# Optimization experiments

Hardware: AMD Instinct MI355X
Metric: run time of the kernel (lower is better)

The kernel has to match this reference:

```python
import jax, jax.numpy as jnp
import numpy as np

B, C, D = 512, 50000, 256
N_LOADED = 40000


def setup_inputs() -> dict:
    key = jax.random.key(0)
    k1, k2, k3, k4 = jax.random.split(key, 4)
    visual_feats = jax.random.normal(k1, (B, D), dtype=jnp.float32)
    text_feats = jax.random.normal(k2, (C, D), dtype=jnp.float32)
    # sparse multi-hot labels; force class 0 positive for every row so the
    # positive set (intersected with loaded ids) is never empty
    batch_label = (jax.random.uniform(k3, (B, C)) < 0.02).astype(jnp.int32)
    batch_label = batch_label.at[:, 0].set(1)
    # distinct loaded class ids; force id 0 to be loaded
    ids = jax.random.permutation(k4, C)[:N_LOADED].astype(jnp.int32)
    ids = jnp.sort(ids).at[0].set(0)
    return {
        "visual_feats": visual_feats,
        "text_feats": text_feats,
        "batch_label": batch_label,
        "class_ids_loaded": ids,
        "d_space": D,
    }


def reference(visual_feats, text_feats, batch_label, class_ids_loaded, d_space):
    num_classes = text_feats.shape[0]
    # membership mask for loaded class ids (the set() intersection in torch)
    loaded = jnp.zeros((num_classes,), dtype=bool).at[class_ids_loaded].set(True)

    # cosine similarity; note: torch adds 1e-6 eps only to text-feature norms
    v = visual_feats / jnp.linalg.norm(visual_feats, axis=1, keepdims=True)
    t = text_feats / (1e-6 + jnp.linalg.norm(text_feats, axis=1, keepdims=True))
    S = v @ t.T  # [B, C]

    pos = (batch_label != 0) & loaded[None, :]  # ragged positive sets, as mask
    neg = (batch_label == 0) & loaded[None, :]  # ragged negative sets, as mask

    # denominator: sum of exp(sim) over negatives, per row
    denom = jnp.sum(jnp.where(neg, jnp.exp(S), 0.0), axis=1)  # [B]
    n_pos = jnp.sum(pos, axis=1).astype(S.dtype)  # [B]

    # per-row loss: mean over positives of -log(exp(s_p)/denom) = log(denom)-s_p
    per_row = jnp.sum(jnp.where(pos, jnp.log(denom)[:, None] - S, 0.0), axis=1) / n_pos
    return jnp.mean(per_row).reshape(1)
```

## Files before the change

### kernel.cpp

```cpp
#include <hip/hip_runtime.h>
#include <math.h>

#define D_DIM 256
#define GTM 64
#define GTN 64
#define BK 32
#define NB 782
#define NBP 784
#define CBPR 4
#define CBLKS (CBPR * 512)

typedef __attribute__((ext_vector_type(8))) short short8;
typedef __attribute__((ext_vector_type(4))) float floatx4;
typedef unsigned long long u64;

__device__ __forceinline__ unsigned short f2bf(float f) {
    unsigned int u = __float_as_uint(f);
    u += 0x7FFFu + ((u >> 16) & 1u);
    return (unsigned short)(u >> 16);
}

__device__ __forceinline__ void gload16(const void* g, void* lds) {
    __builtin_amdgcn_global_load_lds(
        (const __attribute__((address_space(1))) unsigned int*)g,
        (__attribute__((address_space(3))) unsigned int*)lds, 16, 0, 0);
}

__global__ __launch_bounds__(256) void prep_compress(
    const float* __restrict__ V, const float* __restrict__ T,
    const int* __restrict__ label, const int* __restrict__ ids,
    u64* __restrict__ loadedmask, u64* __restrict__ posmask,
    unsigned short* __restrict__ Vb, unsigned short* __restrict__ Tb,
    float* __restrict__ gaccum, unsigned int* __restrict__ gcount,
    int B, int C, int n_loaded, int WPR) {
    const int bid = blockIdx.x;
    const int tid = threadIdx.x;
    const int lane = tid & 63;

    if (bid < CBLKS) {
        __shared__ unsigned char nib[4096];
        int row = bid / CBPR;
        int sub = bid - row * CBPR;
        int cbase = sub * 16384;
        const int* lp = label + (size_t)row * C;
        int4 q[16];
        #pragma unroll
        for (int j = 0; j < 16; ++j) {
            int col = cbase + j * 1024 + tid * 4;
            if (col < C) q[j] = *(const int4*)(lp + col);
            else         q[j] = make_int4(0, 0, 0, 0);
        }
        #pragma unroll
        for (int j = 0; j < 16; ++j) {
            unsigned int n = (q[j].x ? 1u : 0u) | (q[j].y ? 2u : 0u) |
                             (q[j].z ? 4u : 0u) | (q[j].w ? 8u : 0u);
            nib[j * 256 + tid] = (unsigned char)n;
        }
        __syncthreads();
        #pragma unroll
        for (int h = 0; h < 2; ++h) {
            int widx = h * 256 + tid;
            u64 nb8 = *(const u64*)&nib[widx * 8];
            unsigned int word = 0;
            #pragma unroll
            for (int j = 0; j < 8; ++j)
                word |= ((unsigned int)((nb8 >> (8 * j)) & 0xFu)) << (4 * j);
            int u32idx = sub * 512 + widx;
            if (u32idx < 2 * WPR)
                ((unsigned int*)(posmask + (size_t)row * WPR))[u32idx] = word;
        }
        return;
    }

    int ptid = (bid - CBLKS) * 256 + tid;
    if (ptid == 0) { *gcount = 0u; *gaccum = 0.f; }
    if (ptid < WPR) {
        int base = ptid << 6;
        int lo = 0, hi = n_loaded;
        while (lo < hi) { int mid = (lo + hi) >> 1; if (ids[mid] < base) lo = mid + 1; else hi = mid; }
        u64 m = 0;
        for (int i = lo; i < n_loaded; ++i) {
            int v = ids[i]; if (v >= base + 64) break;
            m |= 1ull << (v - base);
        }
        loadedmask[ptid] = m;
    }
    int pwave = (bid - CBLKS) * 4 + (tid >> 6);
    int r0 = pwave * 4;
    if (r0 >= B + C) return;
    float4 x[4];
    #pragma unroll
    for (int q = 0; q < 4; ++q) {
        int wv = r0 + q;
        if (wv < B + C) {
            const float* src = (wv < B) ? (V + (size_t)wv * D_DIM)
                                        : (T + (size_t)(wv - B) * D_DIM);
            x[q] = ((const float4*)src)[lane];
        }
    }
    #pragma unroll
    for (int q = 0; q < 4; ++q) {
        int wv = r0 + q;
        if (wv >= B + C) break;
        bool isV = wv < B;
        float ss = x[q].x * x[q].x + x[q].y * x[q].y + x[q].z * x[q].z + x[q].w * x[q].w;
        #pragma unroll
        for (int off = 32; off > 0; off >>= 1) ss += __shfl_xor(ss, off);
        float nrm = sqrtf(ss);
        float s = isV ? (1.0f / nrm) : (1.0f / (1e-6f + nrm));
        ushort4 o;
        o.x = f2bf(x[q].x * s); o.y = f2bf(x[q].y * s);
        o.z = f2bf(x[q].z * s); o.w = f2bf(x[q].w * s);
        unsigned short* dst = isV ? (Vb + (size_t)wv * D_DIM)
                                  : (Tb + (size_t)(wv - B) * D_DIM);
        ((ushort4*)dst)[lane] = o;
    }
}

__global__ __launch_bounds__(256) void gemm_fused(
    const unsigned short* __restrict__ Vb, const unsigned short* __restrict__ Tb,
    const u64* __restrict__ posmask, const u64* __restrict__ loadedmask,
    float* __restrict__ denomP, float* __restrict__ posP, int C, int WPR) {
    __shared__ unsigned short As[GTM * BK];
    __shared__ unsigned short Bs[GTN * BK];
    __shared__ float sDen[GTM], sPos[GTM];

    const int tid  = threadIdx.x;
    const int lane = tid & 63;
    const int w    = tid >> 6;
    const int m0 = blockIdx.x * GTM;
    const int n0 = blockIdx.y * GTN;

    if (tid < GTM) { sDen[tid] = 0.f; sPos[tid] = 0.f; }

    const int sra = lane >> 2;
    const int kc  = (lane & 3) * 8;
    int ga = m0 + w * 16 + sra;
    int gb = n0 + w * 16 + sra;
    if (gb >= C) gb = C - 1;
    const unsigned short* gA = Vb + (size_t)ga * D_DIM + kc;
    const unsigned short* gB = Tb + (size_t)gb * D_DIM + kc;
    unsigned short* lA = &As[w * 16 * BK];
    unsigned short* lB = &Bs[w * 16 * BK];

    const int wm = (w >> 1) * 32;
    const int wn = (w & 1) * 32;
    const int fr = lane & 15;
    const int quad = lane >> 4;

    floatx4 acc[2][2];
    #pragma unroll
    for (int mi = 0; mi < 2; mi++)
        #pragma unroll
        for (int ni = 0; ni < 2; ni++) acc[mi][ni] = (floatx4)0.f;

    #pragma unroll
    for (int kt = 0; kt < D_DIM / BK; ++kt) {
        if (kt) __syncthreads();
        gload16(gA + kt * BK, lA);
        gload16(gB + kt * BK, lB);
        __syncthreads();
        short8 af[2], bf[2];
        #pragma unroll
        for (int mi = 0; mi < 2; mi++)
            af[mi] = *(const short8*)&As[(wm + mi * 16 + fr) * BK + quad * 8];
        #pragma unroll
        for (int ni = 0; ni < 2; ni++)
            bf[ni] = *(const short8*)&Bs[(wn + ni * 16 + fr) * BK + quad * 8];
        #pragma unroll
        for (int mi = 0; mi < 2; mi++)
            #pragma unroll
            for (int ni = 0; ni < 2; ni++)
                acc[mi][ni] = __builtin_amdgcn_mfma_f32_16x16x32_bf16(
                    af[mi], bf[ni], acc[mi][ni], 0, 0, 0);
    }

    const int wordIdx = n0 >> 6;
    const u64 loadedw = loadedmask[wordIdx];
    #pragma unroll
    for (int mi = 0; mi < 2; mi++) {
        #pragma unroll
        for (int i = 0; i < 4; i++) {
            const int mloc = wm + mi * 16 + quad * 4 + i;
            const u64 praw = posmask[(size_t)(m0 + mloc) * WPR + wordIdx];
            const u64 posw = praw & loadedw;
            const u64 negw = loadedw & ~praw;
            float den = 0.f, pos = 0.f;
            #pragma unroll
            for (int ni = 0; ni < 2; ni++) {
                const float s = acc[mi][ni][i];
                const int bit = wn + ni * 16 + fr;
                if ((negw >> bit) & 1) den += __expf(s);
                if ((posw >> bit) & 1) pos += s;
            }
            #pragma unroll
            for (int off = 8; off >= 1; off >>= 1) {
                den += __shfl_xor(den, off);
                pos += __shfl_xor(pos, off);
            }
            if (fr == 0) {
                if (den != 0.f) atomicAdd(&sDen[mloc], den);
                if (pos != 0.f) atomicAdd(&sPos[mloc], pos);
            }
        }
    }
    __syncthreads();
    if (tid < GTM) {
        denomP[(size_t)(m0 + tid) * NBP + blockIdx.y] = sDen[tid];
        posP[(size_t)(m0 + tid) * NBP + blockIdx.y]   = sPos[tid];
    }
}

__global__ void reduce_rows(const float* __restrict__ denomP, const float* __restrict__ posP,
                            const u64* __restrict__ posmask, const u64* __restrict__ loadedmask,
                            float* __restrict__ gaccum, unsigned int* __restrict__ gcount,
                            float* __restrict__ out, int B, int WPR) {
    __shared__ float bsum[4];
    int wv   = threadIdx.x >> 6;
    int row  = blockIdx.x * 4 + wv;
    int lane = threadIdx.x & 63;
    float den = 0.f, pos = 0.f;
    int cnt = 0;
    if (row < B) {
        for (int bn = lane; bn < NB; bn += 64) {
            den += denomP[(size_t)row * NBP + bn];
            pos += posP[(size_t)row * NBP + bn];
        }
        for (int j = lane; j < WPR; j += 64)
            cnt += __popcll(posmask[(size_t)row * WPR + j] & loadedmask[j]);
        #pragma unroll
        for (int off = 32; off > 0; off >>= 1) {
            den += __shfl_xor(den, off);
            pos += __shfl_xor(pos, off);
            cnt += __shfl_xor(cnt, off);
        }
    }
    if (lane == 0) bsum[wv] = (row < B) ? (logf(den) - pos / (float)cnt) : 0.f;
    __syncthreads();
    if (threadIdx.x == 0) {
        float s = bsum[0] + bsum[1] + bsum[2] + bsum[3];
        atomicAdd(gaccum, s);
        __threadfence();
        unsigned int old = atomicAdd(gcount, 1u);
        if (old == gridDim.x - 1) {
            float tot = atomicAdd(gaccum, 0.0f);
            out[0] = tot / (float)B;
        }
    }
}

extern "C" void kernel_launch(void* const* d_in, const int* in_sizes, int n_in,
                              void* d_out, int out_size, void* d_ws, size_t ws_size,
                              hipStream_t stream) {
    const float* V     = (const float*)d_in[0];
    const float* T     = (const float*)d_in[1];
    const int*   label = (const int*)d_in[2];
    const int*   ids   = (const int*)d_in[3];
    int B = in_sizes[0] / D_DIM;
    int C = in_sizes[1] / D_DIM;
    int n_loaded = in_sizes[3];
    int WPR = (C + 63) >> 6;

    char* ws = (char*)d_ws;
    float*        gaccum = (float*)(ws + 0);
    unsigned int* gcount = (unsigned int*)(ws + 8);
    u64*   loadedmask = (u64*)(ws + 2048);
    u64*   posmask    = (u64*)(ws + 8320);
    unsigned short* Vb = (unsigned short*)(ws + 3211392);
    unsigned short* Tb = (unsigned short*)(ws + 3473536);
    float* denomP  = (float*)(ws + 29073536);
    float* posP    = (float*)(ws + 30679168);

    int prep_waves  = (B + C + 3) / 4;
    int prep_blocks = (prep_waves + 3) / 4;
    prep_compress<<<CBLKS + prep_blocks, 256, 0, stream>>>(
        V, T, label, ids, loadedmask, posmask, Vb, Tb, gaccum, gcount,
        B, C, n_loaded, WPR);

    dim3 grid(B / GTM, NB);
    gemm_fused<<<grid, 256, 0, stream>>>(Vb, Tb, posmask, loadedmask,
                                         denomP, posP, C, WPR);

    reduce_rows<<<(B + 3) / 4, 256, 0, stream>>>(denomP, posP, posmask, loadedmask,
                                                 gaccum, gcount, (float*)d_out, B, WPR);
}
```

Measured before the change: 274.5 us.

## Fuse label bitmask compression into GEMM tiles and count positives in-tile

```diff
diff --git a/kernel.cpp b/kernel.cpp
--- a/kernel.cpp
+++ b/kernel.cpp
@@ -7,8 +7,6 @@
 #define BK 32
 #define NB 782
 #define NBP 784
-#define CBPR 4
-#define CBLKS (CBPR * 512)
 
 typedef __attribute__((ext_vector_type(8))) short short8;
 typedef __attribute__((ext_vector_type(4))) float floatx4;
@@ -26,53 +24,15 @@
         (__attribute__((address_space(3))) unsigned int*)lds, 16, 0, 0);
 }
 
-__global__ __launch_bounds__(256) void prep_compress(
+__global__ __launch_bounds__(256) void prep(
     const float* __restrict__ V, const float* __restrict__ T,
-    const int* __restrict__ label, const int* __restrict__ ids,
-    u64* __restrict__ loadedmask, u64* __restrict__ posmask,
+    const int* __restrict__ ids, u64* __restrict__ loadedmask,
     unsigned short* __restrict__ Vb, unsigned short* __restrict__ Tb,
     float* __restrict__ gaccum, unsigned int* __restrict__ gcount,
     int B, int C, int n_loaded, int WPR) {
-    const int bid = blockIdx.x;
     const int tid = threadIdx.x;
     const int lane = tid & 63;
-
-    if (bid < CBLKS) {
-        __shared__ unsigned char nib[4096];
-        int row = bid / CBPR;
-        int sub = bid - row * CBPR;
-        int cbase = sub * 16384;
-        const int* lp = label + (size_t)row * C;
-        int4 q[16];
-        #pragma unroll
-        for (int j = 0; j < 16; ++j) {
-            int col = cbase + j * 1024 + tid * 4;
-            if (col < C) q[j] = *(const int4*)(lp + col);
-            else         q[j] = make_int4(0, 0, 0, 0);
-        }
-        #pragma unroll
-        for (int j = 0; j < 16; ++j) {
-            unsigned int n = (q[j].x ? 1u : 0u) | (q[j].y ? 2u : 0u) |
-                             (q[j].z ? 4u : 0u) | (q[j].w ? 8u : 0u);
-            nib[j * 256 + tid] = (unsigned char)n;
-        }
-        __syncthreads();
-        #pragma unroll
-        for (int h = 0; h < 2; ++h) {
-            int widx = h * 256 + tid;
-            u64 nb8 = *(const u64*)&nib[widx * 8];
-            unsigned int word = 0;
-            #pragma unroll
-            for (int j = 0; j < 8; ++j)
-                word |= ((unsigned int)((nb8 >> (8 * j)) & 0xFu)) << (4 * j);
-            int u32idx = sub * 512 + widx;
-            if (u32idx < 2 * WPR)
-                ((unsigned int*)(posmask + (size_t)row * WPR))[u32idx] = word;
-        }
-        return;
-    }
-
-    int ptid = (bid - CBLKS) * 256 + tid;
+    int ptid = blockIdx.x * 256 + tid;
     if (ptid == 0) { *gcount = 0u; *gaccum = 0.f; }
     if (ptid < WPR) {
         int base = ptid << 6;
@@ -85,7 +45,7 @@
         }
         loadedmask[ptid] = m;
     }
-    int pwave = (bid - CBLKS) * 4 + (tid >> 6);
+    int pwave = blockIdx.x * 4 + (tid >> 6);
     int r0 = pwave * 4;
     if (r0 >= B + C) return;
     float4 x[4];
@@ -119,11 +79,13 @@
 
 __global__ __launch_bounds__(256) void gemm_fused(
     const unsigned short* __restrict__ Vb, const unsigned short* __restrict__ Tb,
-    const u64* __restrict__ posmask, const u64* __restrict__ loadedmask,
-    float* __restrict__ denomP, float* __restrict__ posP, int C, int WPR) {
+    const int* __restrict__ label, const u64* __restrict__ loadedmask,
+    float* __restrict__ denomP, float* __restrict__ posP, float* __restrict__ npP,
+    int C, int WPR) {
     __shared__ unsigned short As[GTM * BK];
     __shared__ unsigned short Bs[GTN * BK];
-    __shared__ float sDen[GTM], sPos[GTM];
+    __shared__ u64 smask[GTM];
+    __shared__ float sDen[GTM], sPos[GTM], sNp[GTM];
 
     const int tid  = threadIdx.x;
     const int lane = tid & 63;
@@ -131,7 +93,21 @@
     const int m0 = blockIdx.x * GTM;
     const int n0 = blockIdx.y * GTN;
 
-    if (tid < GTM) { sDen[tid] = 0.f; sPos[tid] = 0.f; }
+    if (tid < GTM) { sDen[tid] = 0.f; sPos[tid] = 0.f; sNp[tid] = 0.f; }
+
+    {
+        int col = n0 + lane;
+        if (col >= C) col = C - 1;
+        const int* lp = label + (size_t)(m0 + w * 16) * C + col;
+        int labv[16];
+        #pragma unroll
+        for (int i = 0; i < 16; ++i) labv[i] = lp[(size_t)i * C];
+        #pragma unroll
+        for (int i = 0; i < 16; ++i) {
+            u64 bw = __ballot(labv[i] != 0);
+            if (lane == 0) smask[w * 16 + i] = bw;
+        }
+    }
 
     const int sra = lane >> 2;
     const int kc  = (lane & 3) * 8;
@@ -175,32 +151,32 @@
                     af[mi], bf[ni], acc[mi][ni], 0, 0, 0);
     }
 
-    const int wordIdx = n0 >> 6;
-    const u64 loadedw = loadedmask[wordIdx];
+    const u64 loadedw = loadedmask[n0 >> 6];
     #pragma unroll
     for (int mi = 0; mi < 2; mi++) {
         #pragma unroll
         for (int i = 0; i < 4; i++) {
             const int mloc = wm + mi * 16 + quad * 4 + i;
-            const u64 praw = posmask[(size_t)(m0 + mloc) * WPR + wordIdx];
+            const u64 praw = smask[mloc];
             const u64 posw = praw & loadedw;
             const u64 negw = loadedw & ~praw;
-            float den = 0.f, pos = 0.f;
+            float den = 0.f, pos = 0.f, np = 0.f;
             #pragma unroll
             for (int ni = 0; ni < 2; ni++) {
                 const float s = acc[mi][ni][i];
                 const int bit = wn + ni * 16 + fr;
                 if ((negw >> bit) & 1) den += __expf(s);
-                if ((posw >> bit) & 1) pos += s;
+                if ((posw >> bit) & 1) { pos += s; np += 1.f; }
             }
             #pragma unroll
             for (int off = 8; off >= 1; off >>= 1) {
                 den += __shfl_xor(den, off);
                 pos += __shfl_xor(pos, off);
+                np  += __shfl_xor(np, off);
             }
             if (fr == 0) {
                 if (den != 0.f) atomicAdd(&sDen[mloc], den);
-                if (pos != 0.f) atomicAdd(&sPos[mloc], pos);
+                if (np  != 0.f) { atomicAdd(&sPos[mloc], pos); atomicAdd(&sNp[mloc], np); }
             }
         }
     }
@@ -208,34 +184,33 @@
     if (tid < GTM) {
         denomP[(size_t)(m0 + tid) * NBP + blockIdx.y] = sDen[tid];
         posP[(size_t)(m0 + tid) * NBP + blockIdx.y]   = sPos[tid];
+        npP[(size_t)(m0 + tid) * NBP + blockIdx.y]    = sNp[tid];
     }
 }
 
 __global__ void reduce_rows(const float* __restrict__ denomP, const float* __restrict__ posP,
-                            const u64* __restrict__ posmask, const u64* __restrict__ loadedmask,
+                            const float* __restrict__ npP,
                             float* __restrict__ gaccum, unsigned int* __restrict__ gcount,
-                            float* __restrict__ out, int B, int WPR) {
+                            float* __restrict__ out, int B) {
     __shared__ float bsum[4];
     int wv   = threadIdx.x >> 6;
     int row  = blockIdx.x * 4 + wv;
     int lane = threadIdx.x & 63;
-    float den = 0.f, pos = 0.f;
-    int cnt = 0;
+    float den = 0.f, pos = 0.f, np = 0.f;
     if (row < B) {
         for (int bn = lane; bn < NB; bn += 64) {
             den += denomP[(size_t)row * NBP + bn];
             pos += posP[(size_t)row * NBP + bn];
-        }
-        for (int j = lane; j < WPR; j += 64)
-            cnt += __popcll(posmask[(size_t)row * WPR + j] & loadedmask[j]);
+            np  += npP[(size_t)row * NBP + bn];
+        }
         #pragma unroll
         for (int off = 32; off > 0; off >>= 1) {
             den += __shfl_xor(den, off);
             pos += __shfl_xor(pos, off);
-            cnt += __shfl_xor(cnt, off);
-        }
-    }
-    if (lane == 0) bsum[wv] = (row < B) ? (logf(den) - pos / (float)cnt) : 0.f;
+            np  += __shfl_xor(np, off);
+        }
+    }
+    if (lane == 0) bsum[wv] = (row < B) ? (logf(den) - pos / np) : 0.f;
     __syncthreads();
     if (threadIdx.x == 0) {
         float s = bsum[0] + bsum[1] + bsum[2] + bsum[3];
@@ -265,22 +240,21 @@
     float*        gaccum = (float*)(ws + 0);
     unsigned int* gcount = (unsigned int*)(ws + 8);
     u64*   loadedmask = (u64*)(ws + 2048);
-    u64*   posmask    = (u64*)(ws + 8320);
-    unsigned short* Vb = (unsigned short*)(ws + 3211392);
-    unsigned short* Tb = (unsigned short*)(ws + 3473536);
-    float* denomP  = (float*)(ws + 29073536);
-    float* posP    = (float*)(ws + 30679168);
+    unsigned short* Vb = (unsigned short*)(ws + 8320);
+    unsigned short* Tb = (unsigned short*)(ws + 270464);
+    float* denomP  = (float*)(ws + 25870464);
+    float* posP    = (float*)(ws + 27476096);
+    float* npP     = (float*)(ws + 29081728);
 
     int prep_waves  = (B + C + 3) / 4;
     int prep_blocks = (prep_waves + 3) / 4;
-    prep_compress<<<CBLKS + prep_blocks, 256, 0, stream>>>(
-        V, T, label, ids, loadedmask, posmask, Vb, Tb, gaccum, gcount,
-        B, C, n_loaded, WPR);
+    prep<<<prep_blocks, 256, 0, stream>>>(
+        V, T, ids, loadedmask, Vb, Tb, gaccum, gcount, B, C, n_loaded, WPR);
 
     dim3 grid(B / GTM, NB);
-    gemm_fused<<<grid, 256, 0, stream>>>(Vb, Tb, posmask, loadedmask,
-                                         denomP, posP, C, WPR);
-
-    reduce_rows<<<(B + 3) / 4, 256, 0, stream>>>(denomP, posP, posmask, loadedmask,
-                                                 gaccum, gcount, (float*)d_out, B, WPR);
-}
+    gemm_fused<<<grid, 256, 0, stream>>>(Vb, Tb, label, loadedmask,
+                                         denomP, posP, npP, C, WPR);
+
+    reduce_rows<<<(B + 3) / 4, 256, 0, stream>>>(denomP, posP, npP,
+                                                 gaccum, gcount, (float*)d_out, B);
+}
```

Result: faster. 269.0 us (-2.0%).
